# Performance work log

Measured on AMD Instinct MI355X. Metric: run time of the kernel, lower is better.

The kernel has to match this reference:

```python
import jax, jax.numpy as jnp
import numpy as np

N = 100_000      # nodes
E = 1_600_000    # edges
D = 128          # dim_in == dim_h
L = 3            # num_layers
G = 512          # num graphs in batch
EPS = 1e-5       # BatchNorm1d eps


def setup_inputs() -> dict:
    key = jax.random.key(0)
    k1, k2, k3, k4 = jax.random.split(key, 4)
    x = jax.random.normal(k1, (N, D), dtype=jnp.float32)
    edge_index = jax.random.randint(k2, (2, E), 0, N, dtype=jnp.int64)
    batch = jnp.sort(jax.random.randint(k3, (N,), 0, G, dtype=jnp.int64))
    Ws = jax.random.normal(k4, (L, D, D), dtype=jnp.float32) * 0.05
    bs = jnp.zeros((L, D), dtype=jnp.float32)
    gammas = jnp.ones((L, D), dtype=jnp.float32)
    betas = jnp.zeros((L, D), dtype=jnp.float32)
    return {"x": x, "edge_index": edge_index, "batch": batch,
            "Ws": Ws, "bs": bs, "gammas": gammas, "betas": betas}


def reference(x, edge_index, batch, Ws, bs, gammas, betas):
    src, dst = edge_index[0], edge_index[1]
    # GCN symmetric normalization with self-loops (PyG GCNConv default):
    # deg counts incoming edges at dst, +1 for the self-loop.
    deg = jnp.zeros((N,), dtype=x.dtype).at[dst].add(1.0) + 1.0
    inv_sqrt = jax.lax.rsqrt(deg)
    edge_coeff = inv_sqrt[src] * inv_sqrt[dst]   # [E]
    self_coeff = inv_sqrt * inv_sqrt             # [N] self-loop weight deg^-1

    h = x
    for i in range(L):
        hw = h @ Ws[i]                                           # [N, D]
        agg = (jnp.zeros_like(hw).at[dst].add(hw[src] * edge_coeff[:, None])
               + hw * self_coeff[:, None] + bs[i])               # [N, D]
        # BatchNorm1d (training-mode batch statistics, biased variance)
        mean = agg.mean(axis=0)
        var = agg.var(axis=0)
        hn = (agg - mean) * jax.lax.rsqrt(var + EPS) * gammas[i] + betas[i]
        h = jax.nn.relu(hn)

    # global_add_pool: scatter-add node features by graph id
    return jax.ops.segment_sum(h, batch, num_segments=G)        # [G, D]
```

## Files before the change

### kernel.cpp

```cpp
#include <hip/hip_runtime.h>

#define D 128
#define CHUNK 512
#define NSLICE 8
#define SLW 16

using short8 = __attribute__((ext_vector_type(8))) short;
using f32x4  = __attribute__((ext_vector_type(4))) float;
using f32x2  = __attribute__((ext_vector_type(2))) float;
using u32x2  = __attribute__((ext_vector_type(2))) unsigned;

__device__ __forceinline__ unsigned short f2bf(float f){
  unsigned u = __builtin_bit_cast(unsigned, f);
  u += 0x7fffu + ((u >> 16) & 1u);
  return (unsigned short)(u >> 16);
}
__device__ __forceinline__ float bflo2f(unsigned v){
  return __builtin_bit_cast(float, v << 16);
}
__device__ __forceinline__ float bfhi2f(unsigned v){
  return __builtin_bit_cast(float, v & 0xffff0000u);
}
__device__ __forceinline__ float bfs2f(unsigned short v){
  return __builtin_bit_cast(float, ((unsigned)v) << 16);
}
__device__ __forceinline__ unsigned cvtpk(float lo, float hi){
  unsigned r;
  asm("v_cvt_pk_bf16_f32 %0, %1, %2" : "=v"(r) : "v"(lo), "v"(hi));
  return r;
}

__global__ void k_deg(const int* __restrict__ dst, int* __restrict__ deg,
                      int* __restrict__ rank, int E){
  int e = blockIdx.x * 256 + threadIdx.x;
  if (e < E) rank[e] = atomicAdd(&deg[dst[e]], 1);
}

__global__ void k_chunksum(const int* __restrict__ deg, int* __restrict__ csum, int n){
  __shared__ int s[256];
  int tid = threadIdx.x;
  int n0 = blockIdx.x * CHUNK + tid * 2;
  int v = 0;
  if (n0     < n) v += deg[n0];
  if (n0 + 1 < n) v += deg[n0 + 1];
  s[tid] = v; __syncthreads();
  for (int off = 128; off > 0; off >>= 1){
    if (tid < off) s[tid] += s[tid + off];
    __syncthreads();
  }
  if (tid == 0) csum[blockIdx.x] = s[0];
}

__global__ void k_scanchunks(int* __restrict__ csum, int nchunks){
  __shared__ int s[256];
  int tid = threadIdx.x;
  int v = (tid < nchunks) ? csum[tid] : 0;
  s[tid] = v; __syncthreads();
  for (int off = 1; off < 256; off <<= 1){
    int t = (tid >= off) ? s[tid - off] : 0;
    __syncthreads();
    s[tid] += t;
    __syncthreads();
  }
  if (tid < nchunks) csum[tid] = s[tid] - v;
}

__global__ void k_offsets(const int* __restrict__ deg, const int* __restrict__ csum,
                          int* __restrict__ offs, float* __restrict__ inv, int n){
  __shared__ int s[256];
  int tid = threadIdx.x;
  int n0 = blockIdx.x * CHUNK + tid * 2;
  int d0 = (n0     < n) ? deg[n0]     : 0;
  int d1 = (n0 + 1 < n) ? deg[n0 + 1] : 0;
  int pair = d0 + d1;
  s[tid] = pair; __syncthreads();
  for (int off = 1; off < 256; off <<= 1){
    int t = (tid >= off) ? s[tid - off] : 0;
    __syncthreads();
    s[tid] += t;
    __syncthreads();
  }
  int excl = s[tid] - pair + csum[blockIdx.x];
  if (n0     <= n) offs[n0]     = excl;
  if (n0 + 1 <= n) offs[n0 + 1] = excl + d0;
  if (n0     < n) inv[n0]     = rsqrtf((float)(d0 + 1));
  if (n0 + 1 < n) inv[n0 + 1] = rsqrtf((float)(d1 + 1));
}

__global__ __launch_bounds__(256)
void k_csrfill(const int* __restrict__ src, const int* __restrict__ dst,
               const int* __restrict__ offs, const int* __restrict__ rank,
               int* __restrict__ csrc, int E, int n){
  int part = blockIdx.x & 7;
  int blk  = blockIdx.x >> 3;
  int nblk = gridDim.x >> 3;
  int per = (n + 7) / 8;
  int d0 = part * per, d1 = min(d0 + per, n);
  int stride = nblk * 256;
  for (int e = blk * 256 + threadIdx.x; e < E; e += stride){
    int d = dst[e];
    if (d >= d0 && d < d1){
      csrc[offs[d] + rank[e]] = src[e];
    }
  }
}

#define WSTRIDE 136
__global__ __launch_bounds__(512)
void k_gemm(const float* __restrict__ hf, const unsigned short* __restrict__ hb,
            const float* __restrict__ W, const float* __restrict__ inv,
            const float* __restrict__ scale, const float* __restrict__ shift,
            int do_norm, unsigned short* __restrict__ hwS, int nrows){
  __shared__ unsigned short Wt[128 * WSTRIDE];
  int tid = threadIdx.x;
  for (int i = tid; i < 128 * 128; i += 512){
    int k = i >> 7, c = i & 127;
    Wt[c * WSTRIDE + k] = f2bf(W[i]);
  }
  __syncthreads();

  int wave = tid >> 6, lane = tid & 63;
  int r0 = blockIdx.x * 128 + wave * 16;
  int row = r0 + (lane & 15);
  int kg = lane >> 4;
  int rowc = row < nrows ? row : nrows - 1;

  short8 a[4];
  if (do_norm){
#pragma unroll
    for (int kt = 0; kt < 4; ++kt){
      int k0 = kt * 32 + kg * 8;
      int sl = k0 >> 4, o = k0 & 15;
      short8 raw = *(const short8*)(hb + ((long)sl * nrows + rowc) * SLW + o);
      unsigned u[4];
#pragma unroll
      for (int j = 0; j < 4; ++j){
        float lo = bfs2f((unsigned short)raw[2*j]);
        float hi = bfs2f((unsigned short)raw[2*j+1]);
        lo = fmaxf(0.f, lo * scale[k0+2*j]   + shift[k0+2*j]);
        hi = fmaxf(0.f, hi * scale[k0+2*j+1] + shift[k0+2*j+1]);
        u[j] = cvtpk(lo, hi);
      }
      a[kt] = *(short8*)u;
    }
  } else {
    const float* hrow = hf + (long)rowc * D;
#pragma unroll
    for (int kt = 0; kt < 4; ++kt){
      int k0 = kt * 32 + kg * 8;
      f32x4 v0 = *(const f32x4*)(hrow + k0);
      f32x4 v1 = *(const f32x4*)(hrow + k0 + 4);
      unsigned u[4];
      u[0] = cvtpk(v0[0], v0[1]);
      u[1] = cvtpk(v0[2], v0[3]);
      u[2] = cvtpk(v1[0], v1[1]);
      u[3] = cvtpk(v1[2], v1[3]);
      a[kt] = *(short8*)u;
    }
  }

  f32x4 acc[8] = {};
#pragma unroll
  for (int ct = 0; ct < 8; ++ct){
    int col = ct * 16 + (lane & 15);
    const unsigned short* bp = &Wt[col * WSTRIDE + kg * 8];
#pragma unroll
    for (int kt = 0; kt < 4; ++kt){
      short8 b = *(const short8*)(bp + kt * 32);
      acc[ct] = __builtin_amdgcn_mfma_f32_16x16x32_bf16(a[kt], b, acc[ct], 0, 0, 0);
    }
  }

  int colbase = lane & 15;
  int rowo = r0 + kg * 4;
  float ivr[4];
#pragma unroll
  for (int r = 0; r < 4; ++r) ivr[r] = inv[min(rowo + r, nrows - 1)];
#pragma unroll
  for (int ct = 0; ct < 8; ++ct){
#pragma unroll
    for (int r = 0; r < 4; ++r){
      int rr = rowo + r;
      if (rr < nrows)
        hwS[((long)ct * nrows + rr) * SLW + colbase] = f2bf(acc[ct][r] * ivr[r]);
    }
  }
}

__global__ __launch_bounds__(256)
void k_agg(const unsigned short* __restrict__ hwS, const float* __restrict__ inv,
           const int* __restrict__ offs, const int* __restrict__ csrc,
           const float* __restrict__ bias,
           unsigned* __restrict__ aggS, float* __restrict__ stats, int n,
           int ngroups){
  int g   = blockIdx.x & 7;
  int grp = blockIdx.x >> 3;
  int tid = threadIdx.x, lane = tid & 63, wv = tid >> 6;
  int ns = lane >> 2;
  int cp = lane & 3;
  int nwaves = ngroups * 4;
  int gw = grp * 4 + wv;
  int per = (n + nwaves - 1) / nwaves;
  int n0 = min(gw * per, n), n1 = min(n0 + per, n);

  const u32x2* slice2 = (const u32x2*)((const unsigned*)hwS + (long)g * n * 8);
  u32x2* oslice2 = (u32x2*)(aggS + (long)g * n * 8);

  int cb = g * 16 + cp * 4;
  float b0 = bias[cb], b1 = bias[cb + 1], b2 = bias[cb + 2], b3 = bias[cb + 3];
  float s0 = 0, s1 = 0, s2 = 0, s3 = 0;
  float q0 = 0, q1 = 0, q2 = 0, q3 = 0;

  for (int base = n0; base < n1; base += 16){
    int node = base + ns;
    bool act = node < n1;
    int ndc = act ? node : n1 - 1;
    int e  = offs[ndc];
    int ee = offs[ndc + 1];
    float a0 = 0, a1 = 0, a2 = 0, a3 = 0;

    int i0 = csrc[(e     < ee) ? e     : 0];
    int i1 = csrc[(e + 1 < ee) ? e + 1 : 0];
    int i2 = csrc[(e + 2 < ee) ? e + 2 : 0];
    int i3 = csrc[(e + 3 < ee) ? e + 3 : 0];
    while (__any(e < ee)){
      int j0 = csrc[(e + 4 < ee) ? e + 4 : 0];
      int j1 = csrc[(e + 5 < ee) ? e + 5 : 0];
      int j2 = csrc[(e + 6 < ee) ? e + 6 : 0];
      int j3 = csrc[(e + 7 < ee) ? e + 7 : 0];
      u32x2 v0 = slice2[(long)i0 * 4 + cp];
      u32x2 v1 = slice2[(long)i1 * 4 + cp];
      u32x2 v2 = slice2[(long)i2 * 4 + cp];
      u32x2 v3 = slice2[(long)i3 * 4 + cp];
      bool k0 = e < ee, k1 = e + 1 < ee, k2 = e + 2 < ee, k3 = e + 3 < ee;
      v0[0] = k0 ? v0[0] : 0u; v0[1] = k0 ? v0[1] : 0u;
      v1[0] = k1 ? v1[0] : 0u; v1[1] = k1 ? v1[1] : 0u;
      v2[0] = k2 ? v2[0] : 0u; v2[1] = k2 ? v2[1] : 0u;
      v3[0] = k3 ? v3[0] : 0u; v3[1] = k3 ? v3[1] : 0u;
      a0 += (bflo2f(v0[0]) + bflo2f(v1[0])) + (bflo2f(v2[0]) + bflo2f(v3[0]));
      a1 += (bfhi2f(v0[0]) + bfhi2f(v1[0])) + (bfhi2f(v2[0]) + bfhi2f(v3[0]));
      a2 += (bflo2f(v0[1]) + bflo2f(v1[1])) + (bflo2f(v2[1]) + bflo2f(v3[1]));
      a3 += (bfhi2f(v0[1]) + bfhi2f(v1[1])) + (bfhi2f(v2[1]) + bfhi2f(v3[1]));
      i0 = j0; i1 = j1; i2 = j2; i3 = j3;
      e += 4;
    }

    if (act){
      u32x2 sv = slice2[(long)node * 4 + cp];
      float ivd = inv[node];
      a0 = (a0 + bflo2f(sv[0])) * ivd + b0;
      a1 = (a1 + bfhi2f(sv[0])) * ivd + b1;
      a2 = (a2 + bflo2f(sv[1])) * ivd + b2;
      a3 = (a3 + bfhi2f(sv[1])) * ivd + b3;
      u32x2 pk;
      pk[0] = ((unsigned)f2bf(a1) << 16) | (unsigned)f2bf(a0);
      pk[1] = ((unsigned)f2bf(a3) << 16) | (unsigned)f2bf(a2);
      __builtin_nontemporal_store(pk, oslice2 + (long)node * 4 + cp);
      s0 += a0; s1 += a1; s2 += a2; s3 += a3;
      q0 += a0 * a0; q1 += a1 * a1; q2 += a2 * a2; q3 += a3 * a3;
    }
  }

#pragma unroll
  for (int off = 4; off <= 32; off <<= 1){
    s0 += __shfl_xor(s0, off, 64); s1 += __shfl_xor(s1, off, 64);
    s2 += __shfl_xor(s2, off, 64); s3 += __shfl_xor(s3, off, 64);
    q0 += __shfl_xor(q0, off, 64); q1 += __shfl_xor(q1, off, 64);
    q2 += __shfl_xor(q2, off, 64); q3 += __shfl_xor(q3, off, 64);
  }

  __shared__ float red[4][4][8];
  if (ns == 0){
    red[wv][cp][0] = s0; red[wv][cp][1] = s1;
    red[wv][cp][2] = s2; red[wv][cp][3] = s3;
    red[wv][cp][4] = q0; red[wv][cp][5] = q1;
    red[wv][cp][6] = q2; red[wv][cp][7] = q3;
  }
  __syncthreads();
  if (tid < 4){
    float t[8] = {0,0,0,0,0,0,0,0};
#pragma unroll
    for (int w = 0; w < 4; ++w)
#pragma unroll
      for (int j = 0; j < 8; ++j) t[j] += red[w][tid][j];
    int c = g * 16 + tid * 4;
#pragma unroll
    for (int j = 0; j < 4; ++j){
      atomicAdd(&stats[c + j],       t[j]);
      atomicAdd(&stats[128 + c + j], t[4 + j]);
    }
  }
}

__global__ void k_bn(const float* __restrict__ stats, const float* __restrict__ gamma,
                     const float* __restrict__ beta, float* __restrict__ scale,
                     float* __restrict__ shift, float invn){
  int c = threadIdx.x;
  float mean = stats[c] * invn;
  float var = stats[128 + c] * invn - mean * mean;
  float isd = rsqrtf(var + 1e-5f);
  float sc = gamma[c] * isd;
  scale[c] = sc;
  shift[c] = beta[c] - mean * sc;
}

__global__ __launch_bounds__(256)
void k_pool(const unsigned* __restrict__ aggS, const float* __restrict__ scale,
            const float* __restrict__ shift, const int* __restrict__ batch,
            float* __restrict__ out, int n){
  int tid = threadIdx.x, lane = tid & 63, wv = tid >> 6;
  int gw = blockIdx.x * 4 + wv;
  int n0 = gw * 64;
  if (n0 >= n) return;
  int n1 = min(n0 + 64, n);
  int c0 = lane * 2;
  int sl = lane >> 3, cp = lane & 7;
  long sbase = (long)sl * n * 8;
  float sc0 = scale[c0], sc1 = scale[c0 + 1];
  float sh0 = shift[c0], sh1 = shift[c0 + 1];
  int g = batch[n0];
  float a0 = 0, a1 = 0;
  for (int nd = n0; nd < n1; ++nd){
    int gn = batch[nd];
    if (gn != g){
      atomicAdd(&out[(long)g * D + c0],     a0);
      atomicAdd(&out[(long)g * D + c0 + 1], a1);
      a0 = 0; a1 = 0; g = gn;
    }
    unsigned v = aggS[sbase + (long)nd * 8 + cp];
    a0 += fmaxf(0.f, bflo2f(v) * sc0 + sh0);
    a1 += fmaxf(0.f, bfhi2f(v) * sc1 + sh1);
  }
  atomicAdd(&out[(long)g * D + c0],     a0);
  atomicAdd(&out[(long)g * D + c0 + 1], a1);
}

extern "C" void kernel_launch(void* const* d_in, const int* in_sizes, int n_in,
                              void* d_out, int out_size, void* d_ws, size_t ws_size,
                              hipStream_t stream){
  const float* x      = (const float*)d_in[0];
  const int*   ei     = (const int*)d_in[1];
  const int*   batch  = (const int*)d_in[2];
  const float* Ws     = (const float*)d_in[3];
  const float* bs     = (const float*)d_in[4];
  const float* gammas = (const float*)d_in[5];
  const float* betas  = (const float*)d_in[6];

  const int E_ = in_sizes[1] / 2;
  const int N_ = in_sizes[2];
  const int* src = ei;
  const int* dst = ei + E_;

  char* p = (char*)d_ws;
  auto alloc = [&](size_t bytes) -> void* {
    void* r = (void*)p;
    p += (bytes + 255) & ~(size_t)255;
    return r;
  };
  unsigned*       bufA   = (unsigned*)      alloc((size_t)N_ * D * 2);
  unsigned short* hwS    = (unsigned short*)alloc((size_t)N_ * D * 2);
  int*            deg    = (int*)           alloc((size_t)N_ * 4);
  float*          inv    = (float*)         alloc((size_t)N_ * 4);
  int*            offs   = (int*)           alloc((size_t)(N_ + 1) * 4);
  int*            rank   = (int*)           alloc((size_t)E_ * 4);
  int*            csrc   = (int*)           alloc((size_t)E_ * 4);
  float*          stats  = (float*)         alloc(3 * 256 * 4);
  float*          scales = (float*)         alloc(3 * 128 * 4);
  float*          shifts = (float*)         alloc(3 * 128 * 4);
  int*            csum   = (int*)           alloc(256 * 4);

  hipMemsetAsync(deg,    0, (size_t)N_ * 4, stream);
  hipMemsetAsync(stats,  0, 3 * 256 * 4, stream);
  hipMemsetAsync(d_out,  0, (size_t)out_size * 4, stream);

  int nchunks = (N_ + CHUNK - 1) / CHUNK;
  k_deg       <<<(E_ + 255) / 256, 256, 0, stream>>>(dst, deg, rank, E_);
  k_chunksum  <<<nchunks, 256, 0, stream>>>(deg, csum, N_);
  k_scanchunks<<<1, 256, 0, stream>>>(csum, nchunks);
  k_offsets   <<<nchunks, 256, 0, stream>>>(deg, csum, offs, inv, N_);
  k_csrfill   <<<2048, 256, 0, stream>>>(src, dst, offs, rank, csrc, E_, N_);

  int gemm_blocks = (N_ + 127) / 128;
  int ngroups = 256;
  for (int l = 0; l < 3; ++l){
    const float* sc = (l == 0) ? nullptr : scales + (l - 1) * 128;
    const float* sh = (l == 0) ? nullptr : shifts + (l - 1) * 128;
    k_gemm<<<gemm_blocks, 512, 0, stream>>>(x, (const unsigned short*)bufA,
                                            Ws + (size_t)l * D * D, inv, sc, sh,
                                            (l == 0) ? 0 : 1, hwS, N_);
    k_agg<<<ngroups * 8, 256, 0, stream>>>(hwS, inv, offs, csrc, bs + (size_t)l * D,
                                           bufA, stats + (size_t)l * 256, N_, ngroups);
    k_bn<<<1, 128, 0, stream>>>(stats + (size_t)l * 256, gammas + (size_t)l * D,
                                betas + (size_t)l * D, scales + (size_t)l * 128,
                                shifts + (size_t)l * 128, 1.0f / (float)N_);
  }
  k_pool<<<(N_ + 255) / 256, 256, 0, stream>>>(bufA, scales + 2 * 128, shifts + 2 * 128,
                                               batch, (float*)d_out, N_);
}
```

Baseline: 511.0 us.

## Fold BatchNorm finalize into consumers and stage CSR indices in LDS

Removes the separate k_bn launch by computing BatchNorm scale and shift from the accumulated statistics inside the GEMM and pooling kernels, held in shared memory. In the aggregation kernel, each wave cooperatively loads the neighbor indices of its 16-node chunk into LDS with coalesced reads, then gathers from LDS instead of issuing per-lane dependent global index loads. Chunks with more than ECAP edges fall back to global index reads. This adds LDS usage, which can reduce occupancy, and repeats the tiny BN computation in every block.

Measured after the change: 543.3 us. +6.3%, slower.

```diff
diff --git a/kernel.cpp b/kernel.cpp
--- a/kernel.cpp
+++ b/kernel.cpp
@@ -4,6 +4,7 @@
 #define CHUNK 512
 #define NSLICE 8
 #define SLW 16
+#define ECAP 1024
 
 using short8 = __attribute__((ext_vector_type(8))) short;
 using f32x4  = __attribute__((ext_vector_type(4))) float;
@@ -109,10 +110,20 @@
 __global__ __launch_bounds__(512)
 void k_gemm(const float* __restrict__ hf, const unsigned short* __restrict__ hb,
             const float* __restrict__ W, const float* __restrict__ inv,
-            const float* __restrict__ scale, const float* __restrict__ shift,
+            const float* __restrict__ stats, const float* __restrict__ gamma,
+            const float* __restrict__ beta, float invn,
             int do_norm, unsigned short* __restrict__ hwS, int nrows){
   __shared__ unsigned short Wt[128 * WSTRIDE];
+  __shared__ float s_sc[128], s_sh[128];
   int tid = threadIdx.x;
+  if (do_norm && tid < 128){
+    float mean = stats[tid] * invn;
+    float var = stats[128 + tid] * invn - mean * mean;
+    float isd = rsqrtf(var + 1e-5f);
+    float sc = gamma[tid] * isd;
+    s_sc[tid] = sc;
+    s_sh[tid] = beta[tid] - mean * sc;
+  }
   for (int i = tid; i < 128 * 128; i += 512){
     int k = i >> 7, c = i & 127;
     Wt[c * WSTRIDE + k] = f2bf(W[i]);
@@ -137,8 +148,8 @@
       for (int j = 0; j < 4; ++j){
         float lo = bfs2f((unsigned short)raw[2*j]);
         float hi = bfs2f((unsigned short)raw[2*j+1]);
-        lo = fmaxf(0.f, lo * scale[k0+2*j]   + shift[k0+2*j]);
-        hi = fmaxf(0.f, hi * scale[k0+2*j+1] + shift[k0+2*j+1]);
+        lo = fmaxf(0.f, lo * s_sc[k0+2*j]   + s_sh[k0+2*j]);
+        hi = fmaxf(0.f, hi * s_sc[k0+2*j+1] + s_sh[k0+2*j+1]);
         u[j] = cvtpk(lo, hi);
       }
       a[kt] = *(short8*)u;
@@ -206,43 +217,73 @@
   const u32x2* slice2 = (const u32x2*)((const unsigned*)hwS + (long)g * n * 8);
   u32x2* oslice2 = (u32x2*)(aggS + (long)g * n * 8);
 
+  __shared__ int stg[4][ECAP];
+
   int cb = g * 16 + cp * 4;
   float b0 = bias[cb], b1 = bias[cb + 1], b2 = bias[cb + 2], b3 = bias[cb + 3];
   float s0 = 0, s1 = 0, s2 = 0, s3 = 0;
   float q0 = 0, q1 = 0, q2 = 0, q3 = 0;
 
   for (int base = n0; base < n1; base += 16){
+    int cend = min(base + 16, n1);
+    int eBase = offs[base];
+    int cnt = offs[cend] - eBase;
     int node = base + ns;
     bool act = node < n1;
     int ndc = act ? node : n1 - 1;
     int e  = offs[ndc];
     int ee = offs[ndc + 1];
+    int rel = e - eBase;
+    int len = ee - e;
     float a0 = 0, a1 = 0, a2 = 0, a3 = 0;
 
-    int i0 = csrc[(e     < ee) ? e     : 0];
-    int i1 = csrc[(e + 1 < ee) ? e + 1 : 0];
-    int i2 = csrc[(e + 2 < ee) ? e + 2 : 0];
-    int i3 = csrc[(e + 3 < ee) ? e + 3 : 0];
-    while (__any(e < ee)){
-      int j0 = csrc[(e + 4 < ee) ? e + 4 : 0];
-      int j1 = csrc[(e + 5 < ee) ? e + 5 : 0];
-      int j2 = csrc[(e + 6 < ee) ? e + 6 : 0];
-      int j3 = csrc[(e + 7 < ee) ? e + 7 : 0];
-      u32x2 v0 = slice2[(long)i0 * 4 + cp];
-      u32x2 v1 = slice2[(long)i1 * 4 + cp];
-      u32x2 v2 = slice2[(long)i2 * 4 + cp];
-      u32x2 v3 = slice2[(long)i3 * 4 + cp];
-      bool k0 = e < ee, k1 = e + 1 < ee, k2 = e + 2 < ee, k3 = e + 3 < ee;
-      v0[0] = k0 ? v0[0] : 0u; v0[1] = k0 ? v0[1] : 0u;
-      v1[0] = k1 ? v1[0] : 0u; v1[1] = k1 ? v1[1] : 0u;
-      v2[0] = k2 ? v2[0] : 0u; v2[1] = k2 ? v2[1] : 0u;
-      v3[0] = k3 ? v3[0] : 0u; v3[1] = k3 ? v3[1] : 0u;
-      a0 += (bflo2f(v0[0]) + bflo2f(v1[0])) + (bflo2f(v2[0]) + bflo2f(v3[0]));
-      a1 += (bfhi2f(v0[0]) + bfhi2f(v1[0])) + (bfhi2f(v2[0]) + bfhi2f(v3[0]));
-      a2 += (bflo2f(v0[1]) + bflo2f(v1[1])) + (bflo2f(v2[1]) + bflo2f(v3[1]));
-      a3 += (bfhi2f(v0[1]) + bfhi2f(v1[1])) + (bfhi2f(v2[1]) + bfhi2f(v3[1]));
-      i0 = j0; i1 = j1; i2 = j2; i3 = j3;
-      e += 4;
+    if (cnt <= ECAP){
+      for (int t = lane; t < cnt; t += 64) stg[wv][t] = csrc[eBase + t];
+      int cm1 = cnt - 1;
+      int p = 0;
+      while (__any(p < len)){
+        int i0 = stg[wv][min(rel + p,     cm1)];
+        int i1 = stg[wv][min(rel + p + 1, cm1)];
+        int i2 = stg[wv][min(rel + p + 2, cm1)];
+        int i3 = stg[wv][min(rel + p + 3, cm1)];
+        u32x2 v0 = slice2[(long)i0 * 4 + cp];
+        u32x2 v1 = slice2[(long)i1 * 4 + cp];
+        u32x2 v2 = slice2[(long)i2 * 4 + cp];
+        u32x2 v3 = slice2[(long)i3 * 4 + cp];
+        bool k0 = p < len, k1 = p + 1 < len, k2 = p + 2 < len, k3 = p + 3 < len;
+        v0[0] = k0 ? v0[0] : 0u; v0[1] = k0 ? v0[1] : 0u;
+        v1[0] = k1 ? v1[0] : 0u; v1[1] = k1 ? v1[1] : 0u;
+        v2[0] = k2 ? v2[0] : 0u; v2[1] = k2 ? v2[1] : 0u;
+        v3[0] = k3 ? v3[0] : 0u; v3[1] = k3 ? v3[1] : 0u;
+        a0 += (bflo2f(v0[0]) + bflo2f(v1[0])) + (bflo2f(v2[0]) + bflo2f(v3[0]));
+        a1 += (bfhi2f(v0[0]) + bfhi2f(v1[0])) + (bfhi2f(v2[0]) + bfhi2f(v3[0]));
+        a2 += (bflo2f(v0[1]) + bflo2f(v1[1])) + (bflo2f(v2[1]) + bflo2f(v3[1]));
+        a3 += (bfhi2f(v0[1]) + bfhi2f(v1[1])) + (bfhi2f(v2[1]) + bfhi2f(v3[1]));
+        p += 4;
+      }
+    } else {
+      int cm1 = cnt - 1;
+      int p = 0;
+      while (__any(p < len)){
+        int i0 = csrc[eBase + min(rel + p,     cm1)];
+        int i1 = csrc[eBase + min(rel + p + 1, cm1)];
+        int i2 = csrc[eBase + min(rel + p + 2, cm1)];
+        int i3 = csrc[eBase + min(rel + p + 3, cm1)];
+        u32x2 v0 = slice2[(long)i0 * 4 + cp];
+        u32x2 v1 = slice2[(long)i1 * 4 + cp];
+        u32x2 v2 = slice2[(long)i2 * 4 + cp];
+        u32x2 v3 = slice2[(long)i3 * 4 + cp];
+        bool k0 = p < len, k1 = p + 1 < len, k2 = p + 2 < len, k3 = p + 3 < len;
+        v0[0] = k0 ? v0[0] : 0u; v0[1] = k0 ? v0[1] : 0u;
+        v1[0] = k1 ? v1[0] : 0u; v1[1] = k1 ? v1[1] : 0u;
+        v2[0] = k2 ? v2[0] : 0u; v2[1] = k2 ? v2[1] : 0u;
+        v3[0] = k3 ? v3[0] : 0u; v3[1] = k3 ? v3[1] : 0u;
+        a0 += (bflo2f(v0[0]) + bflo2f(v1[0])) + (bflo2f(v2[0]) + bflo2f(v3[0]));
+        a1 += (bfhi2f(v0[0]) + bfhi2f(v1[0])) + (bfhi2f(v2[0]) + bfhi2f(v3[0]));
+        a2 += (bflo2f(v0[1]) + bflo2f(v1[1])) + (bflo2f(v2[1]) + bflo2f(v3[1]));
+        a3 += (bfhi2f(v0[1]) + bfhi2f(v1[1])) + (bfhi2f(v2[1]) + bfhi2f(v3[1]));
+        p += 4;
+      }
     }
 
     if (act){
@@ -292,23 +333,22 @@
   }
 }
 
-__global__ void k_bn(const float* __restrict__ stats, const float* __restrict__ gamma,
-                     const float* __restrict__ beta, float* __restrict__ scale,
-                     float* __restrict__ shift, float invn){
-  int c = threadIdx.x;
-  float mean = stats[c] * invn;
-  float var = stats[128 + c] * invn - mean * mean;
-  float isd = rsqrtf(var + 1e-5f);
-  float sc = gamma[c] * isd;
-  scale[c] = sc;
-  shift[c] = beta[c] - mean * sc;
-}
-
 __global__ __launch_bounds__(256)
-void k_pool(const unsigned* __restrict__ aggS, const float* __restrict__ scale,
-            const float* __restrict__ shift, const int* __restrict__ batch,
+void k_pool(const unsigned* __restrict__ aggS, const float* __restrict__ stats,
+            const float* __restrict__ gamma, const float* __restrict__ beta,
+            float invn, const int* __restrict__ batch,
             float* __restrict__ out, int n){
+  __shared__ float psc[128], psh[128];
   int tid = threadIdx.x, lane = tid & 63, wv = tid >> 6;
+  if (tid < 128){
+    float mean = stats[tid] * invn;
+    float var = stats[128 + tid] * invn - mean * mean;
+    float isd = rsqrtf(var + 1e-5f);
+    float sc = gamma[tid] * isd;
+    psc[tid] = sc;
+    psh[tid] = beta[tid] - mean * sc;
+  }
+  __syncthreads();
   int gw = blockIdx.x * 4 + wv;
   int n0 = gw * 64;
   if (n0 >= n) return;
@@ -316,8 +356,8 @@
   int c0 = lane * 2;
   int sl = lane >> 3, cp = lane & 7;
   long sbase = (long)sl * n * 8;
-  float sc0 = scale[c0], sc1 = scale[c0 + 1];
-  float sh0 = shift[c0], sh1 = shift[c0 + 1];
+  float sc0 = psc[c0], sc1 = psc[c0 + 1];
+  float sh0 = psh[c0], sh1 = psh[c0 + 1];
   int g = batch[n0];
   float a0 = 0, a1 = 0;
   for (int nd = n0; nd < n1; ++nd){
@@ -365,14 +405,13 @@
   int*            rank   = (int*)           alloc((size_t)E_ * 4);
   int*            csrc   = (int*)           alloc((size_t)E_ * 4);
   float*          stats  = (float*)         alloc(3 * 256 * 4);
-  float*          scales = (float*)         alloc(3 * 128 * 4);
-  float*          shifts = (float*)         alloc(3 * 128 * 4);
   int*            csum   = (int*)           alloc(256 * 4);
 
   hipMemsetAsync(deg,    0, (size_t)N_ * 4, stream);
   hipMemsetAsync(stats,  0, 3 * 256 * 4, stream);
   hipMemsetAsync(d_out,  0, (size_t)out_size * 4, stream);
 
+  float invn = 1.0f / (float)N_;
   int nchunks = (N_ + CHUNK - 1) / CHUNK;
   k_deg       <<<(E_ + 255) / 256, 256, 0, stream>>>(dst, deg, rank, E_);
   k_chunksum  <<<nchunks, 256, 0, stream>>>(deg, csum, N_);
@@ -383,17 +422,17 @@
   int gemm_blocks = (N_ + 127) / 128;
   int ngroups = 256;
   for (int l = 0; l < 3; ++l){
-    const float* sc = (l == 0) ? nullptr : scales + (l - 1) * 128;
-    const float* sh = (l == 0) ? nullptr : shifts + (l - 1) * 128;
+    const float* st = (l == 0) ? stats : stats + (size_t)(l - 1) * 256;
+    const float* gm = (l == 0) ? gammas : gammas + (size_t)(l - 1) * D;
+    const float* bt = (l == 0) ? betas : betas + (size_t)(l - 1) * D;
     k_gemm<<<gemm_blocks, 512, 0, stream>>>(x, (const unsigned short*)bufA,
-                                            Ws + (size_t)l * D * D, inv, sc, sh,
+                                            Ws + (size_t)l * D * D, inv,
+                                            st, gm, bt, invn,
                                             (l == 0) ? 0 : 1, hwS, N_);
     k_agg<<<ngroups * 8, 256, 0, stream>>>(hwS, inv, offs, csrc, bs + (size_t)l * D,
                                            bufA, stats + (size_t)l * 256, N_, ngroups);
-    k_bn<<<1, 128, 0, stream>>>(stats + (size_t)l * 256, gammas + (size_t)l * D,
-                                betas + (size_t)l * D, scales + (size_t)l * 128,
-                                shifts + (size_t)l * 128, 1.0f / (float)N_);
-  }
-  k_pool<<<(N_ + 255) / 256, 256, 0, stream>>>(bufA, scales + 2 * 128, shifts + 2 * 128,
+  }
+  k_pool<<<(N_ + 255) / 256, 256, 0, stream>>>(bufA, stats + 2 * 256,
+                                               gammas + 2 * D, betas + 2 * D, invn,
                                                batch, (float*)d_out, N_);
 }
```
